# Kernel tuning notes

Hardware: AMD Instinct MI355X
Metric: run time of the kernel (lower is better)

Reference implementation:

```python
import jax, jax.numpy as jnp
import numpy as np

N_NODES = 8192
N_EDGES = 262144
D_FEAT = 512
NHID = 32
LATENT = 16


def setup_inputs() -> dict:
    key = jax.random.key(0)
    ks = jax.random.split(key, 12)
    inp = {
        "features": jax.random.normal(ks[0], (N_NODES, D_FEAT), dtype=jnp.float32),
        "edge_src": jax.random.randint(ks[1], (N_EDGES,), 0, N_NODES, dtype=jnp.int32),
        "edge_dst": jax.random.randint(ks[2], (N_EDGES,), 0, N_NODES, dtype=jnp.int32),
        "edge_weight": jax.random.uniform(ks[3], (N_EDGES,), dtype=jnp.float32),
        # GCEncoder params (GCNConv: out = A @ (x W) + b)
        "Wg1": jax.random.normal(ks[4], (D_FEAT, NHID), dtype=jnp.float32) / np.sqrt(D_FEAT),
        "bg1": jnp.zeros((NHID,), jnp.float32),
        "Wg2": jax.random.normal(ks[5], (NHID, LATENT), dtype=jnp.float32) / np.sqrt(NHID),
        "bg2": jnp.zeros((LATENT,), jnp.float32),
        # MLP encoder params
        "We1": jax.random.normal(ks[6], (D_FEAT, NHID), dtype=jnp.float32) / np.sqrt(D_FEAT),
        "be1": jnp.zeros((NHID,), jnp.float32),
        "We2": jax.random.normal(ks[7], (NHID, LATENT), dtype=jnp.float32) / np.sqrt(NHID),
        "be2": jnp.zeros((LATENT,), jnp.float32),
        # MLP decoder params (latent -> features)
        "Wd1": jax.random.normal(ks[8], (LATENT, NHID), dtype=jnp.float32) / np.sqrt(LATENT),
        "bd1": jnp.zeros((NHID,), jnp.float32),
        "Wd2": jax.random.normal(ks[9], (NHID, D_FEAT), dtype=jnp.float32) / np.sqrt(NHID),
        "bd2": jnp.zeros((D_FEAT,), jnp.float32),
    }
    return inp


def _gcn_conv(x, W, b, edge_src, edge_dst, edge_weight, n_nodes):
    # transform then sparse aggregate: A @ (x W) + b
    xw = x @ W                                   # [N, out]
    msg = xw[edge_src] * edge_weight[:, None]    # [E, out]
    agg = jax.ops.segment_sum(msg, edge_dst, num_segments=n_nodes)
    return agg + b


def reference(features, edge_src, edge_dst, edge_weight,
              Wg1, bg1, Wg2, bg2, We1, be1, We2, be2, Wd1, bd1, Wd2, bd2):
    n = features.shape[0]
    # GCEncoder (dropout p=0.0)
    h = jax.nn.relu(_gcn_conv(features, Wg1, bg1, edge_src, edge_dst, edge_weight, n))
    za = jax.nn.relu(_gcn_conv(h, Wg2, bg2, edge_src, edge_dst, edge_weight, n))
    # MLP encoder
    zx = jax.nn.relu(jax.nn.relu(features @ We1 + be1) @ We2 + be2)
    # concat latents
    z = jnp.concatenate([za, zx], axis=1)        # [N, 2*latent]
    # inner-product decoder: sigmoid(z z^T)  -> [N, N]
    adj_recon = jax.nn.sigmoid(z @ z.T)
    # feature decoder MLP
    feat_recon = jax.nn.relu(jax.nn.relu(zx @ Wd1 + bd1) @ Wd2 + bd2)
    return adj_recon, feat_recon, z
```

## Files before the change

kernel.cpp:

```cpp
#include <hip/hip_runtime.h>

typedef unsigned short ushort_t;
typedef __attribute__((ext_vector_type(8))) short short8;
typedef __attribute__((ext_vector_type(4))) float floatx4;
typedef __attribute__((ext_vector_type(2))) float floatx2;

#define N_NODES 8192
#define N_EDGES 262144
#define D_FEAT 512
#define NHID 32
#define LATENT 16

#define ADJ_OFF 0
#define FEAT_OFF (8192*8192)
#define Z_OFF (8192*8192 + 8192*512)

static __device__ __forceinline__ ushort_t f2bf(float f) {
    unsigned int u = __float_as_uint(f);
    unsigned int r = u + 0x7fffu + ((u >> 16) & 1u);
    return (ushort_t)(r >> 16);
}

static __device__ __forceinline__ float fsig(float x) {
    float e = __builtin_amdgcn_exp2f(x * -1.44269504f);
    return __builtin_amdgcn_rcpf(1.f + e);
}

__global__ __launch_bounds__(256) void k_enc(const float* __restrict__ feat,
                                             const float* __restrict__ Wg1,
                                             const float* __restrict__ We1,
                                             const float* __restrict__ be1,
                                             const float* __restrict__ We2,
                                             const float* __restrict__ be2,
                                             float* __restrict__ xwg,
                                             float* __restrict__ zxf,
                                             int* __restrict__ counts) {
    __shared__ float WL[32][64];
    __shared__ float FL[16][36];
    __shared__ float HE[16][33];
    int tid = threadIdx.x;
    int gid = blockIdx.x * 256 + tid;
    if (gid < N_NODES) counts[gid] = 0;

    int n = tid >> 4;
    int cr = tid & 15;
    int m0 = blockIdx.x * 16;
    float acc[4] = {};

    for (int kt = 0; kt < 16; kt++) {
        __syncthreads();
        {
            int i = tid;
            #pragma unroll
            for (int j = 0; j < 8; j++, i += 256) {
                int k = i >> 6, c = i & 63;
                int kg = kt * 32 + k;
                WL[k][c] = (c < 32) ? Wg1[kg * 32 + c] : We1[kg * 32 + (c - 32)];
            }
        }
        if (tid < 128) {
            int nn = tid >> 3, q = tid & 7;
            float4 v = *(const float4*)(feat + (m0 + nn) * 512 + kt * 32 + q * 4);
            FL[nn][q * 4 + 0] = v.x; FL[nn][q * 4 + 1] = v.y;
            FL[nn][q * 4 + 2] = v.z; FL[nn][q * 4 + 3] = v.w;
        }
        __syncthreads();
        #pragma unroll 4
        for (int k = 0; k < 32; k++) {
            float4 w = *(const float4*)&WL[k][cr * 4];
            float f0 = FL[n][k];
            acc[0] += f0 * w.x; acc[1] += f0 * w.y;
            acc[2] += f0 * w.z; acc[3] += f0 * w.w;
        }
    }
    int cg = cr * 4;
    if (cg < 32) {
        float4 v = make_float4(acc[0], acc[1], acc[2], acc[3]);
        *(float4*)(xwg + (m0 + n) * 32 + cg) = v;
    } else {
        int hc = cg - 32;
        #pragma unroll
        for (int t = 0; t < 4; t++) {
            float v = acc[t] + be1[hc + t];
            HE[n][hc + t] = v > 0.f ? v : 0.f;
        }
    }
    __syncthreads();
    {
        int j = cr;
        float s = be2[j];
        #pragma unroll 8
        for (int cc = 0; cc < 32; cc++) s += HE[n][cc] * We2[cc * 16 + j];
        zxf[(m0 + n) * 16 + j] = s > 0.f ? s : 0.f;
    }
}

__global__ __launch_bounds__(256) void k_hist(const int* __restrict__ edst, int* __restrict__ counts) {
    int e = blockIdx.x * 256 + threadIdx.x;
    atomicAdd(&counts[edst[e]], 1);
}

__global__ __launch_bounds__(1024) void k_scan(const int* __restrict__ counts,
                                               int* __restrict__ offs, int* __restrict__ cursor) {
    __shared__ int sdata[1024];
    int t = threadIdx.x;
    int base = t * 8;
    int c[8], local[8];
    int s = 0;
    #pragma unroll
    for (int j = 0; j < 8; j++) { c[j] = counts[base + j]; }
    #pragma unroll
    for (int j = 0; j < 8; j++) { local[j] = s; s += c[j]; }
    sdata[t] = s;
    __syncthreads();
    for (int off = 1; off < 1024; off <<= 1) {
        int v = sdata[t];
        int add = (t >= off) ? sdata[t - off] : 0;
        __syncthreads();
        sdata[t] = v + add;
        __syncthreads();
    }
    int excl = (t == 0) ? 0 : sdata[t - 1];
    #pragma unroll
    for (int j = 0; j < 8; j++) {
        int o = excl + local[j];
        offs[base + j] = o;
        cursor[base + j] = o;
    }
}

__global__ __launch_bounds__(256) void k_scatter(const int* __restrict__ esrc,
                                                 const int* __restrict__ edst,
                                                 const float* __restrict__ ew,
                                                 int* __restrict__ cursor,
                                                 int2* __restrict__ sedge) {
    int e = blockIdx.x * 256 + threadIdx.x;
    int d = edst[e];
    int pos = atomicAdd(&cursor[d], 1);
    sedge[pos] = make_int2(esrc[e], __float_as_int(ew[e]));
}

__global__ __launch_bounds__(256) void k_agg1(const float* __restrict__ xwg,
                                              const int* __restrict__ offs,
                                              const int* __restrict__ counts,
                                              const int2* __restrict__ sedge,
                                              const float* __restrict__ bg1,
                                              const float* __restrict__ Wg2,
                                              float* __restrict__ hw2) {
    __shared__ float hsh[8][33];
    int ln = threadIdx.x >> 5, c = threadIdx.x & 31;
    int n = blockIdx.x * 8 + ln;
    int st = offs[n], en = st + counts[n];
    float acc = 0.f;
    int i = st;
    for (; i + 4 <= en; i += 4) {
        int2 e0 = sedge[i], e1 = sedge[i + 1], e2 = sedge[i + 2], e3 = sedge[i + 3];
        float s0 = __int_as_float(e0.y) * xwg[e0.x * 32 + c];
        float s1 = __int_as_float(e1.y) * xwg[e1.x * 32 + c];
        float s2 = __int_as_float(e2.y) * xwg[e2.x * 32 + c];
        float s3 = __int_as_float(e3.y) * xwg[e3.x * 32 + c];
        acc += (s0 + s1) + (s2 + s3);
    }
    for (; i < en; i++) {
        int2 e = sedge[i];
        acc += __int_as_float(e.y) * xwg[e.x * 32 + c];
    }
    float h = acc + bg1[c];
    hsh[ln][c] = h > 0.f ? h : 0.f;
    __syncthreads();
    if (threadIdx.x < 128) {
        int l2 = threadIdx.x >> 4, j = threadIdx.x & 15;
        float s2 = 0.f;
        #pragma unroll 8
        for (int cc = 0; cc < 32; cc++) s2 += hsh[l2][cc] * Wg2[cc * 16 + j];
        hw2[(blockIdx.x * 8 + l2) * 16 + j] = s2;
    }
}

__global__ __launch_bounds__(256) void k_agg2(const float* __restrict__ hw2,
                                              const int* __restrict__ offs,
                                              const int* __restrict__ counts,
                                              const int2* __restrict__ sedge,
                                              const float* __restrict__ bg2,
                                              const float* __restrict__ zxf,
                                              ushort_t* __restrict__ zbf,
                                              float* __restrict__ zout) {
    int ln = threadIdx.x >> 4, c = threadIdx.x & 15;
    int n = blockIdx.x * 16 + ln;
    int st = offs[n], en = st + counts[n];
    float acc = 0.f;
    int i = st;
    for (; i + 4 <= en; i += 4) {
        int2 e0 = sedge[i], e1 = sedge[i + 1], e2 = sedge[i + 2], e3 = sedge[i + 3];
        float s0 = __int_as_float(e0.y) * hw2[e0.x * 16 + c];
        float s1 = __int_as_float(e1.y) * hw2[e1.x * 16 + c];
        float s2 = __int_as_float(e2.y) * hw2[e2.x * 16 + c];
        float s3 = __int_as_float(e3.y) * hw2[e3.x * 16 + c];
        acc += (s0 + s1) + (s2 + s3);
    }
    for (; i < en; i++) {
        int2 e = sedge[i];
        acc += __int_as_float(e.y) * hw2[e.x * 16 + c];
    }
    float za = acc + bg2[c];
    za = za > 0.f ? za : 0.f;
    float zx = zxf[n * 16 + c];
    zout[n * 32 + c] = za;
    zout[n * 32 + 16 + c] = zx;
    zbf[n * 32 + c] = f2bf(za);
    zbf[n * 32 + 16 + c] = f2bf(zx);
}

__global__ __launch_bounds__(256) void k_out(const ushort_t* __restrict__ zbf,
                                             const float* __restrict__ zxf,
                                             const float* __restrict__ Wd1,
                                             const float* __restrict__ bd1,
                                             const float* __restrict__ Wd2,
                                             const float* __restrict__ bd2,
                                             float* __restrict__ out) {
    __shared__ float ZL[16][17];
    __shared__ float HT[16][33];
    int tid = threadIdx.x;
    if (blockIdx.x < 2048) {
        float* adj = out + ADJ_OFF;
        int l = tid & 63;
        int wv = tid >> 6;
        int strip = blockIdx.x & 15;
        int rt = (blockIdx.x >> 4) * 4 + wv;
        int q = l >> 4, cl = l & 15;
        int m0 = rt * 16, c0 = strip * 512;
        short8 a = *(const short8*)(zbf + (m0 + cl) * 32 + q * 8);
        for (int g = 0; g < 8; g++) {
            int cb = c0 + g * 64;
            short8 b0 = *(const short8*)(zbf + (cb + 4 * cl + 0) * 32 + q * 8);
            short8 b1 = *(const short8*)(zbf + (cb + 4 * cl + 1) * 32 + q * 8);
            short8 b2 = *(const short8*)(zbf + (cb + 4 * cl + 2) * 32 + q * 8);
            short8 b3 = *(const short8*)(zbf + (cb + 4 * cl + 3) * 32 + q * 8);
            floatx4 zv = {0, 0, 0, 0};
            floatx4 a0 = __builtin_amdgcn_mfma_f32_16x16x32_bf16(a, b0, zv, 0, 0, 0);
            floatx4 a1 = __builtin_amdgcn_mfma_f32_16x16x32_bf16(a, b1, zv, 0, 0, 0);
            floatx4 a2 = __builtin_amdgcn_mfma_f32_16x16x32_bf16(a, b2, zv, 0, 0, 0);
            floatx4 a3 = __builtin_amdgcn_mfma_f32_16x16x32_bf16(a, b3, zv, 0, 0, 0);
            #pragma unroll
            for (int r = 0; r < 4; r++) {
                floatx4 v;
                v.x = fsig(a0[r]);
                v.y = fsig(a1[r]);
                v.z = fsig(a2[r]);
                v.w = fsig(a3[r]);
                int row = m0 + q * 4 + r;
                *(floatx4*)(adj + (size_t)row * 8192 + cb + 4 * cl) = v;
            }
        }
    } else {
        float* outF = out + FEAT_OFF;
        int m0 = (blockIdx.x - 2048) * 16;
        {
            int n = tid >> 4, k = tid & 15;
            ZL[n][k] = zxf[(m0 + n) * 16 + k];
        }
        __syncthreads();
        {
            int o = tid * 2;
            int n = o >> 5, c = o & 31;
            float s0 = bd1[c], s1 = bd1[c + 1];
            #pragma unroll
            for (int k = 0; k < 16; k++) {
                float z = ZL[n][k];
                s0 += z * Wd1[k * 32 + c];
                s1 += z * Wd1[k * 32 + c + 1];
            }
            HT[n][c] = s0 > 0.f ? s0 : 0.f;
            HT[n][c + 1] = s1 > 0.f ? s1 : 0.f;
        }
        __syncthreads();
        int c2 = tid * 2;
        floatx2 acc[16];
        #pragma unroll
        for (int n = 0; n < 16; n++) acc[n] = (floatx2){0.f, 0.f};
        for (int k = 0; k < 32; k++) {
            float2 w = *(const float2*)(Wd2 + k * 512 + c2);
            #pragma unroll
            for (int n = 0; n < 16; n++) {
                float t = HT[n][k];
                acc[n].x += t * w.x;
                acc[n].y += t * w.y;
            }
        }
        float b0 = bd2[c2], b1 = bd2[c2 + 1];
        #pragma unroll
        for (int n = 0; n < 16; n++) {
            float s0 = acc[n].x + b0, s1 = acc[n].y + b1;
            s0 = s0 > 0.f ? s0 : 0.f;
            s1 = s1 > 0.f ? s1 : 0.f;
            floatx2 pk = {s0, s1};
            *(floatx2*)(outF + (size_t)(m0 + n) * 512 + c2) = pk;
        }
    }
}

extern "C" void kernel_launch(void* const* d_in, const int* in_sizes, int n_in,
                              void* d_out, int out_size, void* d_ws, size_t ws_size,
                              hipStream_t stream) {
    const float* feat = (const float*)d_in[0];
    const int* esrc = (const int*)d_in[1];
    const int* edst = (const int*)d_in[2];
    const float* ew = (const float*)d_in[3];
    const float* Wg1 = (const float*)d_in[4];
    const float* bg1 = (const float*)d_in[5];
    const float* Wg2 = (const float*)d_in[6];
    const float* bg2 = (const float*)d_in[7];
    const float* We1 = (const float*)d_in[8];
    const float* be1 = (const float*)d_in[9];
    const float* We2 = (const float*)d_in[10];
    const float* be2 = (const float*)d_in[11];
    const float* Wd1 = (const float*)d_in[12];
    const float* bd1 = (const float*)d_in[13];
    const float* Wd2 = (const float*)d_in[14];
    const float* bd2 = (const float*)d_in[15];
    float* out = (float*)d_out;

    char* ws = (char*)d_ws;
    float* xwg      = (float*)(ws + 0);
    float* zxf      = (float*)(ws + 1048576);
    float* hw2      = (float*)(ws + 1572864);
    ushort_t* zbf   = (ushort_t*)(ws + 2097152);
    int* counts     = (int*)(ws + 2621440);
    int* offs       = (int*)(ws + 2654208);
    int* cursor     = (int*)(ws + 2686976);
    int2* sedge     = (int2*)(ws + 2719744);

    k_enc<<<N_NODES / 16, 256, 0, stream>>>(feat, Wg1, We1, be1, We2, be2,
                                            xwg, zxf, counts);
    k_hist<<<N_EDGES / 256, 256, 0, stream>>>(edst, counts);
    k_scan<<<1, 1024, 0, stream>>>(counts, offs, cursor);
    k_scatter<<<N_EDGES / 256, 256, 0, stream>>>(esrc, edst, ew, cursor, sedge);
    k_agg1<<<N_NODES / 8, 256, 0, stream>>>(xwg, offs, counts, sedge, bg1, Wg2, hw2);
    k_agg2<<<N_NODES / 16, 256, 0, stream>>>(hw2, offs, counts, sedge, bg2, zxf,
                                             zbf, out + Z_OFF);
    k_out<<<2048 + 512, 256, 0, stream>>>(zbf, zxf, Wd1, bd1, Wd2, bd2, out);
}
```

Before: 447.3 us.

## Stage adjacency tiles in LDS for coalesced nontemporal stores; move feature decoder earlier

The adjacency kernel now computes sigmoid tiles into shared memory and writes whole contiguous row segments with nontemporal stores, replacing the scattered 16-byte-per-lane stores. The goal is better write coalescing and less cache pollution on the 256 MB output. The feature decoder MLP moves into the edge-scatter kernel so it runs alongside the scatter, leaving the final kernel purely write-bound. The trade-off is extra shared-memory traffic and barriers in the adjacency kernel, plus smaller 128-thread blocks.

```diff
diff --git a/kernel.cpp b/kernel.cpp
--- a/kernel.cpp
+++ b/kernel.cpp
@@ -129,15 +129,69 @@
     }
 }
 
-__global__ __launch_bounds__(256) void k_scatter(const int* __restrict__ esrc,
-                                                 const int* __restrict__ edst,
-                                                 const float* __restrict__ ew,
-                                                 int* __restrict__ cursor,
-                                                 int2* __restrict__ sedge) {
-    int e = blockIdx.x * 256 + threadIdx.x;
-    int d = edst[e];
-    int pos = atomicAdd(&cursor[d], 1);
-    sedge[pos] = make_int2(esrc[e], __float_as_int(ew[e]));
+__global__ __launch_bounds__(256) void k_scatfeat(const int* __restrict__ esrc,
+                                                  const int* __restrict__ edst,
+                                                  const float* __restrict__ ew,
+                                                  int* __restrict__ cursor,
+                                                  int2* __restrict__ sedge,
+                                                  const float* __restrict__ zxf,
+                                                  const float* __restrict__ Wd1,
+                                                  const float* __restrict__ bd1,
+                                                  const float* __restrict__ Wd2,
+                                                  const float* __restrict__ bd2,
+                                                  float* __restrict__ outF) {
+    __shared__ float ZL[16][17];
+    __shared__ float HT[16][33];
+    int tid = threadIdx.x;
+    if (blockIdx.x < 1024) {
+        int e = blockIdx.x * 256 + tid;
+        int d = edst[e];
+        int pos = atomicAdd(&cursor[d], 1);
+        sedge[pos] = make_int2(esrc[e], __float_as_int(ew[e]));
+    } else {
+        int m0 = (int)(blockIdx.x - 1024) * 16;
+        {
+            int n = tid >> 4, k = tid & 15;
+            ZL[n][k] = zxf[(m0 + n) * 16 + k];
+        }
+        __syncthreads();
+        {
+            int o = tid * 2;
+            int n = o >> 5, c = o & 31;
+            float s0 = bd1[c], s1 = bd1[c + 1];
+            #pragma unroll
+            for (int k = 0; k < 16; k++) {
+                float z = ZL[n][k];
+                s0 += z * Wd1[k * 32 + c];
+                s1 += z * Wd1[k * 32 + c + 1];
+            }
+            HT[n][c] = s0 > 0.f ? s0 : 0.f;
+            HT[n][c + 1] = s1 > 0.f ? s1 : 0.f;
+        }
+        __syncthreads();
+        int c2 = tid * 2;
+        floatx2 acc[16];
+        #pragma unroll
+        for (int n = 0; n < 16; n++) acc[n] = (floatx2){0.f, 0.f};
+        for (int k = 0; k < 32; k++) {
+            float2 w = *(const float2*)(Wd2 + k * 512 + c2);
+            #pragma unroll
+            for (int n = 0; n < 16; n++) {
+                float t = HT[n][k];
+                acc[n].x += t * w.x;
+                acc[n].y += t * w.y;
+            }
+        }
+        float b0 = bd2[c2], b1 = bd2[c2 + 1];
+        #pragma unroll
+        for (int n = 0; n < 16; n++) {
+            float s0 = acc[n].x + b0, s1 = acc[n].y + b1;
+            s0 = s0 > 0.f ? s0 : 0.f;
+            s1 = s1 > 0.f ? s1 : 0.f;
+            floatx2 pk = {s0, s1};
+            *(floatx2*)(outF + (size_t)(m0 + n) * 512 + c2) = pk;
+        }
+    }
 }
 
 __global__ __launch_bounds__(256) void k_agg1(const float* __restrict__ xwg,
@@ -211,27 +265,25 @@
     zbf[n * 32 + 16 + c] = f2bf(zx);
 }
 
-__global__ __launch_bounds__(256) void k_out(const ushort_t* __restrict__ zbf,
-                                             const float* __restrict__ zxf,
-                                             const float* __restrict__ Wd1,
-                                             const float* __restrict__ bd1,
-                                             const float* __restrict__ Wd2,
-                                             const float* __restrict__ bd2,
-                                             float* __restrict__ out) {
-    __shared__ float ZL[16][17];
-    __shared__ float HT[16][33];
+__global__ __launch_bounds__(128) void k_adj(const ushort_t* __restrict__ zbf,
+                                             float* __restrict__ adj) {
+    __shared__ float TB[2][16][256];
     int tid = threadIdx.x;
-    if (blockIdx.x < 2048) {
-        float* adj = out + ADJ_OFF;
-        int l = tid & 63;
-        int wv = tid >> 6;
-        int strip = blockIdx.x & 15;
-        int rt = (blockIdx.x >> 4) * 4 + wv;
-        int q = l >> 4, cl = l & 15;
-        int m0 = rt * 16, c0 = strip * 512;
-        short8 a = *(const short8*)(zbf + (m0 + cl) * 32 + q * 8);
-        for (int g = 0; g < 8; g++) {
-            int cb = c0 + g * 64;
+    int l = tid & 63;
+    int wv = tid >> 6;
+    int strip = blockIdx.x & 15;
+    int rt = (blockIdx.x >> 4) * 2 + wv;
+    int q = l >> 4, cl = l & 15;
+    int m0 = rt * 16, c0 = strip * 512;
+    float (*T)[256] = TB[wv];
+
+    short8 a = *(const short8*)(zbf + (m0 + cl) * 32 + q * 8);
+    for (int half = 0; half < 2; half++) {
+        int cb0 = c0 + half * 256;
+        __syncthreads();
+        #pragma unroll
+        for (int g = 0; g < 4; g++) {
+            int cb = cb0 + g * 64;
             short8 b0 = *(const short8*)(zbf + (cb + 4 * cl + 0) * 32 + q * 8);
             short8 b1 = *(const short8*)(zbf + (cb + 4 * cl + 1) * 32 + q * 8);
             short8 b2 = *(const short8*)(zbf + (cb + 4 * cl + 2) * 32 + q * 8);
@@ -248,53 +300,14 @@
                 v.y = fsig(a1[r]);
                 v.z = fsig(a2[r]);
                 v.w = fsig(a3[r]);
-                int row = m0 + q * 4 + r;
-                *(floatx4*)(adj + (size_t)row * 8192 + cb + 4 * cl) = v;
+                *(floatx4*)&T[q * 4 + r][g * 64 + 4 * cl] = v;
             }
         }
-    } else {
-        float* outF = out + FEAT_OFF;
-        int m0 = (blockIdx.x - 2048) * 16;
-        {
-            int n = tid >> 4, k = tid & 15;
-            ZL[n][k] = zxf[(m0 + n) * 16 + k];
-        }
-        __syncthreads();
-        {
-            int o = tid * 2;
-            int n = o >> 5, c = o & 31;
-            float s0 = bd1[c], s1 = bd1[c + 1];
-            #pragma unroll
-            for (int k = 0; k < 16; k++) {
-                float z = ZL[n][k];
-                s0 += z * Wd1[k * 32 + c];
-                s1 += z * Wd1[k * 32 + c + 1];
-            }
-            HT[n][c] = s0 > 0.f ? s0 : 0.f;
-            HT[n][c + 1] = s1 > 0.f ? s1 : 0.f;
-        }
-        __syncthreads();
-        int c2 = tid * 2;
-        floatx2 acc[16];
-        #pragma unroll
-        for (int n = 0; n < 16; n++) acc[n] = (floatx2){0.f, 0.f};
-        for (int k = 0; k < 32; k++) {
-            float2 w = *(const float2*)(Wd2 + k * 512 + c2);
-            #pragma unroll
-            for (int n = 0; n < 16; n++) {
-                float t = HT[n][k];
-                acc[n].x += t * w.x;
-                acc[n].y += t * w.y;
-            }
-        }
-        float b0 = bd2[c2], b1 = bd2[c2 + 1];
-        #pragma unroll
-        for (int n = 0; n < 16; n++) {
-            float s0 = acc[n].x + b0, s1 = acc[n].y + b1;
-            s0 = s0 > 0.f ? s0 : 0.f;
-            s1 = s1 > 0.f ? s1 : 0.f;
-            floatx2 pk = {s0, s1};
-            *(floatx2*)(outF + (size_t)(m0 + n) * 512 + c2) = pk;
+        __syncthreads();
+        #pragma unroll 4
+        for (int r = 0; r < 16; r++) {
+            floatx4 v = *(const floatx4*)&T[r][4 * l];
+            __builtin_nontemporal_store(v, (floatx4*)(adj + (size_t)(m0 + r) * 8192 + cb0 + 4 * l));
         }
     }
 }
@@ -334,9 +347,10 @@
                                             xwg, zxf, counts);
     k_hist<<<N_EDGES / 256, 256, 0, stream>>>(edst, counts);
     k_scan<<<1, 1024, 0, stream>>>(counts, offs, cursor);
-    k_scatter<<<N_EDGES / 256, 256, 0, stream>>>(esrc, edst, ew, cursor, sedge);
+    k_scatfeat<<<1024 + 512, 256, 0, stream>>>(esrc, edst, ew, cursor, sedge,
+                                               zxf, Wd1, bd1, Wd2, bd2, out + FEAT_OFF);
     k_agg1<<<N_NODES / 8, 256, 0, stream>>>(xwg, offs, counts, sedge, bg1, Wg2, hw2);
     k_agg2<<<N_NODES / 16, 256, 0, stream>>>(hw2, offs, counts, sedge, bg2, zxf,
                                              zbf, out + Z_OFF);
-    k_out<<<2048 + 512, 256, 0, stream>>>(zbf, zxf, Wd1, bd1, Wd2, bd2, out);
-}
+    k_adj<<<(N_NODES / 16 / 2) * 16, 128, 0, stream>>>(zbf, out + ADJ_OFF);
+}
```

Result: faster. 438.4 us (-2.0%).
